# Optimization experiments

Measured on AMD Instinct MI355X. Metric: run time of the kernel, lower is better.

## Reference

```python
import jax, jax.numpy as jnp
import numpy as np

B, S, C, H, W = 8, 64, 3, 224, 224   # batch, n_segments, channels, height, width
E, P = 128, 16                        # embed_dim, patch size of feature extractor


def _conv(x, w, b, stride, padding):
    y = jax.lax.conv_general_dilated(
        x, w, (stride, stride), padding,
        dimension_numbers=('NCHW', 'OIHW', 'NCHW'))
    return y + b[None, :, None, None]


def setup_inputs() -> dict:
    key = jax.random.key(0)
    k1, k2, k3 = jax.random.split(key, 3)
    img = jax.random.normal(k1, (B, C, H, W), jnp.float32)
    # SpixelNet stand-in: 3x3 conv -> n_segments logit channels
    w_spixel = jax.random.normal(k2, (S, C, 3, 3), jnp.float32) * 0.1
    b_spixel = jnp.zeros((S,), jnp.float32)
    # feature extractor stand-in: 16x16/16 patch conv -> embed_dim, then GAP
    w_patch = jax.random.normal(k3, (E, C, P, P), jnp.float32) * 0.02
    b_patch = jnp.zeros((E,), jnp.float32)
    return dict(img=img, w_spixel=w_spixel, b_spixel=b_spixel,
                w_patch=w_patch, b_patch=b_patch)


def reference(img, w_spixel, b_spixel, w_patch, b_patch):
    # superpixel tokenizer -> segment logits, argmax -> hard labels
    logits = _conv(img, w_spixel, b_spixel, 1, 'SAME')          # [B,S,H,W]
    labels = jnp.argmax(logits, axis=1)                          # [B,H,W] int

    # replicate per-batch torch.unique (sorted unique labels, zero-padded)
    flat = labels.reshape(B, -1)
    present = jnp.zeros((B, S), bool).at[jnp.arange(B)[:, None], flat].set(True)
    vals = jnp.where(present, jnp.arange(S)[None, :], S)
    uniq = jnp.sort(vals, axis=1)                                # uniques first
    uniq = jnp.where(uniq < S, uniq, 0)                          # pad with 0 like torch.zeros

    # broadcast-compare mask build + masked extract (the memory-bound op)
    mask = (labels[:, None, :, :] == uniq[:, :, None, None]).astype(img.dtype)  # [B,S,H,W]
    seg = (img[:, None, :, :, :] * mask[:, :, None, :, :]).reshape(B * S, C, H, W)

    # feature extractor: patch conv + global average pool
    feat = _conv(seg, w_patch, b_patch, P, 'VALID')              # [B*S,E,H/P,W/P]
    feat = feat.mean(axis=(2, 3))                                # [B*S,E]
    return feat.reshape(B, S, E)
```

## Files before the change

### kernel.cpp

```cpp
#include <hip/hip_runtime.h>

#define BD 8
#define SD 64
#define CD 3
#define HD 224
#define WD 224
#define ED 128
#define PD 16
#define HWD (HD*WD)
#define KD (CD*PD*PD)
#define PRT 8
#define CHK (HWD/PRT)
#define IG 4

typedef float v2f __attribute__((ext_vector_type(2)));

__device__ float              g_part[BD * CD * PRT * SD * 256];
__device__ int                g_labels[BD * HWD];
__device__ unsigned long long g_ppres[BD * PRT];

__global__ __launch_bounds__(256) void k_labels(
    const float* __restrict__ img,
    const float* __restrict__ wsp,
    const float* __restrict__ bsp)
{
    __shared__ __align__(16) float4 w_s[16 * 28];
    const int tid = threadIdx.x;
    for (int t = tid; t < 16 * 28; t += 256) {
        const int q = t / 28, j = t - q * 28;
        float4 v;
        if (j < 27) {
            v.x = wsp[(4 * q + 0) * 27 + j];
            v.y = wsp[(4 * q + 1) * 27 + j];
            v.z = wsp[(4 * q + 2) * 27 + j];
            v.w = wsp[(4 * q + 3) * 27 + j];
        } else {
            v.x = bsp[4 * q + 0]; v.y = bsp[4 * q + 1];
            v.z = bsp[4 * q + 2]; v.w = bsp[4 * q + 3];
        }
        w_s[t] = v;
    }
    __syncthreads();

    const int p = blockIdx.x * 256 + tid;
    const int b = blockIdx.y;
    const int h = p / WD;
    const int w = p - h * WD;

    const float* ib = img + (size_t)b * CD * HWD;
    v2f pd[27];
    #pragma unroll
    for (int c = 0; c < 3; ++c)
        #pragma unroll
        for (int dh = 0; dh < 3; ++dh)
            #pragma unroll
            for (int dw = 0; dw < 3; ++dw) {
                int hh = h + dh - 1, ww = w + dw - 1;
                bool ok = (hh >= 0) & (hh < HD) & (ww >= 0) & (ww < WD);
                const float val = ok ? ib[c * HWD + hh * WD + ww] : 0.f;
                const int j = (c * 3 + dh) * 3 + dw;
                pd[j].x = val; pd[j].y = val;
            }

    float best = -INFINITY;
    int bi = 0;
    for (int q = 0; q < 16; ++q) {
        const float4* wrow = w_s + q * 28;
        const float4 bq = wrow[27];
        v2f a01 = { bq.x, bq.y };
        v2f a23 = { bq.z, bq.w };
        #pragma unroll
        for (int j = 0; j < 27; ++j) {
            const float4 wv = wrow[j];
            const v2f w01 = { wv.x, wv.y };
            const v2f w23 = { wv.z, wv.w };
            a01 = __builtin_elementwise_fma(pd[j], w01, a01);
            a23 = __builtin_elementwise_fma(pd[j], w23, a23);
        }
        if (a01.x > best) { best = a01.x; bi = 4 * q;     }
        if (a01.y > best) { best = a01.y; bi = 4 * q + 1; }
        if (a23.x > best) { best = a23.x; bi = 4 * q + 2; }
        if (a23.y > best) { best = a23.y; bi = 4 * q + 3; }
    }
    g_labels[b * HWD + p] = bi;
}

__global__ __launch_bounds__(256) void k_hist(const float* __restrict__ img)
{
    const int part = blockIdx.x, c = blockIdx.y, b = blockIdx.z;
    const int tid = threadIdx.x;

    __shared__ float acc[SD * 256];
    __shared__ unsigned long long pm;
    #pragma unroll
    for (int k = 0; k < 16; ++k)
        ((float4*)acc)[k * 256 + tid] = make_float4(0.f, 0.f, 0.f, 0.f);
    if (tid == 0) pm = 0ull;
    __syncthreads();

    const int start = part * CHK;
    const int*   lb = g_labels + (size_t)b * HWD;
    const float* ic = img + ((size_t)b * CD + c) * HWD;

    unsigned long long m = 0ull;

    #define HIST_GROUP(g)                                                  \
    {                                                                      \
        const int p4 = start + (g) * 4;                                    \
        const int4   l4 = *(const int4*)(lb + p4);                         \
        const float4 v4 = *(const float4*)(ic + p4);                       \
        const int h = p4 / WD;                                             \
        const int w0 = p4 - h * WD;                                        \
        const int base = ((h & 15) << 4) | (w0 & 15);                      \
        atomicAdd(&acc[l4.x * 256 + base + 0], v4.x);                      \
        atomicAdd(&acc[l4.y * 256 + base + 1], v4.y);                      \
        atomicAdd(&acc[l4.z * 256 + base + 2], v4.z);                      \
        atomicAdd(&acc[l4.w * 256 + base + 3], v4.w);                      \
        m |= 1ull << l4.x; m |= 1ull << l4.y;                              \
        m |= 1ull << l4.z; m |= 1ull << l4.w;                              \
    }

    #pragma unroll
    for (int it = 0; it < 6; ++it) HIST_GROUP(tid + it * 256);
    if (tid < (CHK / 4 - 6 * 256)) HIST_GROUP(tid + 6 * 256);
    #undef HIST_GROUP

    #pragma unroll
    for (int d = 1; d < 64; d <<= 1) m |= __shfl_xor(m, d, 64);
    if ((tid & 63) == 0) atomicOr(&pm, m);
    __syncthreads();

    float4* dst = (float4*)(g_part + (((size_t)(b * CD + c)) * PRT + part) * (SD * 256));
    #pragma unroll
    for (int k = 0; k < 16; ++k)
        dst[k * 256 + tid] = ((float4*)acc)[k * 256 + tid];
    if (c == 0 && tid == 0) g_ppres[b * PRT + part] = pm;
}

__global__ __launch_bounds__(256) void k_out(
    const float* __restrict__ wp,
    const float* __restrict__ bp,
    float* __restrict__ out)
{
    __shared__ float4 gs4[IG][KD / 4];
    const int ig = blockIdx.x;
    const int b = blockIdx.y;
    const int z = blockIdx.z;
    const int tid = threadIdx.x;
    const int lane = tid & 63;
    const int wv = tid >> 6;

    unsigned long long m = 0ull;
    #pragma unroll
    for (int p2 = 0; p2 < PRT; ++p2) m |= g_ppres[b * PRT + p2];
    const int nu = __popcll(m);

    int ls[IG];
    #pragma unroll
    for (int ii = 0; ii < IG; ++ii) {
        const int i = ig * IG + ii;
        int l = 0;
        if (i < nu) {
            unsigned long long mm = m;
            for (int t = 0; t < i; ++t) mm &= mm - 1;
            l = __builtin_ctzll(mm);
        }
        ls[ii] = l;
    }

    #pragma unroll
    for (int k = 0; k < 3; ++k) {
        const int t = tid + k * 256;
        const int ii_ = t / 192, idx = t - ii_ * 192;
        const int c = idx >> 6, cell4 = idx & 63;
        const float4* src = (const float4*)g_part
            + ((size_t)(b * CD + c) * PRT) * 4096 + ls[ii_] * 64 + cell4;
        float4 s = src[0];
        #pragma unroll
        for (int p2 = 1; p2 < PRT; ++p2) {
            float4 v = src[(size_t)p2 * 4096];
            s.x += v.x; s.y += v.y; s.z += v.z; s.w += v.w;
        }
        gs4[ii_][idx] = s;
    }
    __syncthreads();

    float4 G[IG][3];
    #pragma unroll
    for (int ii = 0; ii < IG; ++ii) {
        G[ii][0] = gs4[ii][lane];
        G[ii][1] = gs4[ii][lane + 64];
        G[ii][2] = gs4[ii][lane + 128];
    }

    #pragma unroll 2
    for (int j = 0; j < 8; ++j) {
        const int e = z * 32 + wv * 8 + j;
        const float4* wr = (const float4*)(wp + (size_t)e * KD);
        const float4 a0 = wr[lane], a1 = wr[lane + 64], a2 = wr[lane + 128];
        float acc[IG];
        #pragma unroll
        for (int ii = 0; ii < IG; ++ii) {
            float t = G[ii][0].x * a0.x;
            t = fmaf(G[ii][0].y, a0.y, t); t = fmaf(G[ii][0].z, a0.z, t);
            t = fmaf(G[ii][0].w, a0.w, t);
            t = fmaf(G[ii][1].x, a1.x, t); t = fmaf(G[ii][1].y, a1.y, t);
            t = fmaf(G[ii][1].z, a1.z, t); t = fmaf(G[ii][1].w, a1.w, t);
            t = fmaf(G[ii][2].x, a2.x, t); t = fmaf(G[ii][2].y, a2.y, t);
            t = fmaf(G[ii][2].z, a2.z, t); t = fmaf(G[ii][2].w, a2.w, t);
            acc[ii] = t;
        }
        #pragma unroll
        for (int off = 32; off; off >>= 1) {
            #pragma unroll
            for (int ii = 0; ii < IG; ++ii) acc[ii] += __shfl_xor(acc[ii], off, 64);
        }
        if (lane == 0) {
            #pragma unroll
            for (int ii = 0; ii < IG; ++ii)
                out[(size_t)(b * SD + ig * IG + ii) * ED + e] = bp[e] + acc[ii] * (1.f / 196.f);
        }
    }
}

extern "C" void kernel_launch(void* const* d_in, const int* in_sizes, int n_in,
                              void* d_out, int out_size, void* d_ws, size_t ws_size,
                              hipStream_t stream) {
    const float *img = nullptr, *wsp = nullptr, *bsp = nullptr, *wp = nullptr, *bp = nullptr;
    for (int i = 0; i < n_in; ++i) {
        switch (in_sizes[i]) {
            case BD * CD * HWD:      img = (const float*)d_in[i]; break;
            case SD * CD * 9:        wsp = (const float*)d_in[i]; break;
            case SD:                 bsp = (const float*)d_in[i]; break;
            case ED * CD * PD * PD:  wp  = (const float*)d_in[i]; break;
            case ED:                 bp  = (const float*)d_in[i]; break;
        }
    }
    float* out = (float*)d_out;

    dim3 g1(HWD / 256, BD, 1);
    k_labels<<<g1, 256, 0, stream>>>(img, wsp, bsp);

    dim3 g2(PRT, CD, BD);
    k_hist<<<g2, 256, 0, stream>>>(img);

    dim3 g3(SD / IG, BD, 4);
    k_out<<<g3, 256, 0, stream>>>(wp, bp, out);
}
```

Baseline: 120.1 us.

## Compute four vertical pixels per thread in label conv to reuse loads and weights

The 3x3 conv plus argmax kernel now has each thread produce labels for four vertically adjacent pixels. It loads a 6-row input window once per channel and reuses each shared-memory weight read across all four pixels, cutting global loads and LDS traffic per pixel. The grid shrinks fourfold, to about 392 blocks, which lowers parallelism and raises register pressure. An FMA order swap in the output kernel is incidental.

```diff
diff --git a/kernel.cpp b/kernel.cpp
--- a/kernel.cpp
+++ b/kernel.cpp
@@ -42,47 +42,74 @@
     }
     __syncthreads();
 
-    const int p = blockIdx.x * 256 + tid;
+    const int pp = blockIdx.x * 256 + tid;
     const int b = blockIdx.y;
-    const int h = p / WD;
-    const int w = p - h * WD;
+    const int hp = pp / WD;
+    const int w  = pp - hp * WD;
+    const int h0 = 4 * hp;
 
     const float* ib = img + (size_t)b * CD * HWD;
-    v2f pd[27];
+    float va[3][6][3];
     #pragma unroll
     for (int c = 0; c < 3; ++c)
         #pragma unroll
+        for (int rr = 0; rr < 6; ++rr)
+            #pragma unroll
+            for (int dw = 0; dw < 3; ++dw) {
+                const int hh = h0 - 1 + rr, ww = w + dw - 1;
+                const bool ok = (hh >= 0) & (hh < HD) & (ww >= 0) & (ww < WD);
+                va[c][rr][dw] = ok ? ib[c * HWD + hh * WD + ww] : 0.f;
+            }
+
+    v2f pAB[27], pCD[27];
+    #pragma unroll
+    for (int c = 0; c < 3; ++c)
+        #pragma unroll
         for (int dh = 0; dh < 3; ++dh)
             #pragma unroll
             for (int dw = 0; dw < 3; ++dw) {
-                int hh = h + dh - 1, ww = w + dw - 1;
-                bool ok = (hh >= 0) & (hh < HD) & (ww >= 0) & (ww < WD);
-                const float val = ok ? ib[c * HWD + hh * WD + ww] : 0.f;
                 const int j = (c * 3 + dh) * 3 + dw;
-                pd[j].x = val; pd[j].y = val;
+                pAB[j].x = va[c][dh + 0][dw]; pAB[j].y = va[c][dh + 1][dw];
+                pCD[j].x = va[c][dh + 2][dw]; pCD[j].y = va[c][dh + 3][dw];
             }
 
-    float best = -INFINITY;
-    int bi = 0;
+    float bestA = -INFINITY, bestB = -INFINITY, bestC = -INFINITY, bestD = -INFINITY;
+    int biA = 0, biB = 0, biC = 0, biD = 0;
     for (int q = 0; q < 16; ++q) {
         const float4* wrow = w_s + q * 28;
         const float4 bq = wrow[27];
-        v2f a01 = { bq.x, bq.y };
-        v2f a23 = { bq.z, bq.w };
+        v2f aAB[4], aCD[4];
+        aAB[0] = (v2f){bq.x, bq.x}; aCD[0] = (v2f){bq.x, bq.x};
+        aAB[1] = (v2f){bq.y, bq.y}; aCD[1] = (v2f){bq.y, bq.y};
+        aAB[2] = (v2f){bq.z, bq.z}; aCD[2] = (v2f){bq.z, bq.z};
+        aAB[3] = (v2f){bq.w, bq.w}; aCD[3] = (v2f){bq.w, bq.w};
         #pragma unroll
         for (int j = 0; j < 27; ++j) {
             const float4 wv = wrow[j];
-            const v2f w01 = { wv.x, wv.y };
-            const v2f w23 = { wv.z, wv.w };
-            a01 = __builtin_elementwise_fma(pd[j], w01, a01);
-            a23 = __builtin_elementwise_fma(pd[j], w23, a23);
-        }
-        if (a01.x > best) { best = a01.x; bi = 4 * q;     }
-        if (a01.y > best) { best = a01.y; bi = 4 * q + 1; }
-        if (a23.x > best) { best = a23.x; bi = 4 * q + 2; }
-        if (a23.y > best) { best = a23.y; bi = 4 * q + 3; }
-    }
-    g_labels[b * HWD + p] = bi;
+            const v2f w0 = {wv.x, wv.x}, w1 = {wv.y, wv.y};
+            const v2f w2 = {wv.z, wv.z}, w3 = {wv.w, wv.w};
+            aAB[0] = __builtin_elementwise_fma(pAB[j], w0, aAB[0]);
+            aCD[0] = __builtin_elementwise_fma(pCD[j], w0, aCD[0]);
+            aAB[1] = __builtin_elementwise_fma(pAB[j], w1, aAB[1]);
+            aCD[1] = __builtin_elementwise_fma(pCD[j], w1, aCD[1]);
+            aAB[2] = __builtin_elementwise_fma(pAB[j], w2, aAB[2]);
+            aCD[2] = __builtin_elementwise_fma(pCD[j], w2, aCD[2]);
+            aAB[3] = __builtin_elementwise_fma(pAB[j], w3, aAB[3]);
+            aCD[3] = __builtin_elementwise_fma(pCD[j], w3, aCD[3]);
+        }
+        #pragma unroll
+        for (int k = 0; k < 4; ++k) {
+            if (aAB[k].x > bestA) { bestA = aAB[k].x; biA = 4 * q + k; }
+            if (aAB[k].y > bestB) { bestB = aAB[k].y; biB = 4 * q + k; }
+            if (aCD[k].x > bestC) { bestC = aCD[k].x; biC = 4 * q + k; }
+            if (aCD[k].y > bestD) { bestD = aCD[k].y; biD = 4 * q + k; }
+        }
+    }
+    int* lrow = g_labels + b * HWD + h0 * WD + w;
+    lrow[0 * WD] = biA;
+    lrow[1 * WD] = biB;
+    lrow[2 * WD] = biC;
+    lrow[3 * WD] = biD;
 }
 
 __global__ __launch_bounds__(256) void k_hist(const float* __restrict__ img)
@@ -207,7 +234,7 @@
             t = fmaf(G[ii][1].x, a1.x, t); t = fmaf(G[ii][1].y, a1.y, t);
             t = fmaf(G[ii][1].z, a1.z, t); t = fmaf(G[ii][1].w, a1.w, t);
             t = fmaf(G[ii][2].x, a2.x, t); t = fmaf(G[ii][2].y, a2.y, t);
-            t = fmaf(G[ii][2].z, a2.z, t); t = fmaf(G[ii][2].w, a2.w, t);
+            t = fmaf(G[ii][2].w, a2.w, t); t = fmaf(G[ii][2].z, a2.z, t);
             acc[ii] = t;
         }
         #pragma unroll
@@ -238,7 +265,7 @@
     }
     float* out = (float*)d_out;
 
-    dim3 g1(HWD / 256, BD, 1);
+    dim3 g1(HWD / 1024, BD, 1);
     k_labels<<<g1, 256, 0, stream>>>(img, wsp, bsp);
 
     dim3 g2(PRT, CD, BD);
```

Result: faster. 113.9 us (-5.1%).
